# Optimization experiments

Measured on AMD Instinct MI355X. Metric: run time of the kernel, lower is better.

The kernel has to match this reference:

```python
import jax, jax.numpy as jnp
import numpy as np

TAU = 2.0      # membrane time constant
V_TH = 1.0     # spike threshold (v_reset = 0, hard reset)
T_STEPS = 4    # num_steps

@jax.custom_vjp
def heaviside_atan(x):
    # forward: Heaviside; backward: spikingjelly ATan surrogate (alpha=2)
    return (x >= 0.0).astype(x.dtype)

def _h_fwd(x):
    return heaviside_atan(x), x

def _h_bwd(x, g):
    alpha = 2.0
    return (g * (alpha / 2.0) / (1.0 + (jnp.pi / 2.0 * alpha * x) ** 2),)

heaviside_atan.defvjp(_h_fwd, _h_bwd)

def lif_multistep(x_seq):
    # spikingjelly LIFNode, step_mode='m', decay_input=True, v_reset=0, detach_reset=True
    def step(v, x):
        v = v + (x - v) / TAU                      # charge
        s = heaviside_atan(v - V_TH)               # fire (surrogate grad)
        v = v * (1.0 - jax.lax.stop_gradient(s))   # hard reset, detached spike
        return v, s
    v0 = jnp.zeros_like(x_seq[0])
    _, spikes = jax.lax.scan(step, v0, x_seq)
    return spikes

def setup_inputs() -> dict:
    key = jax.random.key(0)
    k0, k1, k2 = jax.random.split(key, 3)
    B, L, C, D, NL = 16, 512, 128, 1024, 2
    inputs = jax.random.normal(k0, (B, L, C), jnp.float32)
    enc_W = jax.random.normal(k1, (C, D), jnp.float32) / np.sqrt(C).astype(np.float32)
    enc_b = jnp.zeros((D,), jnp.float32)
    W_cells = jax.random.normal(k2, (NL, D, D), jnp.float32) / np.sqrt(D).astype(np.float32)
    b_cells = jnp.zeros((NL, D), jnp.float32)
    return {"inputs": inputs, "enc_W": enc_W, "enc_b": enc_b,
            "W_cells": W_cells, "b_cells": b_cells}

def reference(inputs, enc_W, enc_b, W_cells, b_cells):
    # temporal spike encoder: repeat input over T steps, LIF-encode to spikes
    x = jnp.swapaxes(inputs, 1, 2)                       # [B, C, L]
    x = jnp.broadcast_to(x[None], (T_STEPS,) + x.shape)  # [T, B, C, L]
    h = lif_multistep(x)
    h = jnp.swapaxes(h, -2, -1)                          # [T, B, L, C]
    # encoder linear + init LIF
    h = lif_multistep(h @ enc_W + enc_b)                 # [T, B, L, D]
    # stacked SpikeRNNCells: Linear(D,D) -> multistep LIF
    for i in range(W_cells.shape[0]):
        h = lif_multistep(h @ W_cells[i] + b_cells[i])
    out = h.mean(0)                                      # [B, L, D]
    return out, out.mean(axis=1)                         # ([B,L,D], [B,D])
```

## Files before the change

### kernel.cpp

```cpp
#include <hip/hip_runtime.h>
#include <hip/hip_bf16.h>
#include <stdint.h>

#define TSTEPS 4

typedef __bf16 bf16_t;
typedef __attribute__((ext_vector_type(8))) __bf16 bf16x8;
typedef __attribute__((ext_vector_type(16))) float f32x16;
typedef __attribute__((ext_vector_type(4))) unsigned short ushort4v;

union frag_u { bf16x8 v; uint32_t d[4]; unsigned short u[8]; };

#define WT_VM5      0xF75
#define WT_VM5_LG0  0x075
#define WT_VM4_LG0  0x074
#define WT_VM0_LG0  0x070


__global__ void spike_encode_i8(const float* __restrict__ x,
                                uint4* __restrict__ s1)
{
    const int C = 128;
    int tid = blockIdx.x * blockDim.x + threadIdx.x;
    int row = tid & 31;
    int kb  = (tid >> 5) & 7;
    int m_blk = tid >> 8;
    int m = m_blk * 32 + row;
    const float* px = x + (size_t)m * C + kb * 16;
    float xv[16];
#pragma unroll
    for (int j = 0; j < 16; j += 4) {
        float4 t4 = *(const float4*)(px + j);
        xv[j] = t4.x; xv[j+1] = t4.y; xv[j+2] = t4.z; xv[j+3] = t4.w;
    }
    float v[16];
#pragma unroll
    for (int j = 0; j < 16; ++j) v[j] = 0.0f;
#pragma unroll
    for (int t = 0; t < TSTEPS; ++t) {
        uint32_t dw[4] = {0u, 0u, 0u, 0u};
#pragma unroll
        for (int j = 0; j < 16; ++j) {
            float vv = __fadd_rn(v[j], __fmul_rn(__fsub_rn(xv[j], v[j]), 0.5f));
            bool sp = (vv >= 1.0f);
            dw[j >> 2] |= sp ? (0x3Fu << ((j & 3) * 8)) : 0u;
            v[j] = sp ? 0.0f : vv;
        }
        uint4 o; o.x = dw[0]; o.y = dw[1]; o.z = dw[2]; o.w = dw[3];
        s1[((size_t)(m_blk * 8 + kb) * 4 + t) * 32 + row] = o;
    }
}

__global__ void split_transpose_all(const float* __restrict__ enc_W,
                                    const float* __restrict__ W_cells,
                                    bf16_t* __restrict__ W1h, bf16_t* __restrict__ W1l,
                                    bf16_t* __restrict__ W2h, bf16_t* __restrict__ W2l,
                                    bf16_t* __restrict__ W3h, bf16_t* __restrict__ W3l)
{
    const int N = 1024;
    const float* W;
    bf16_t *hi, *lo;
    int K;
    if (blockIdx.z == 0) {
        if (blockIdx.x >= 4) return;
        W = enc_W; hi = W1h; lo = W1l; K = 128;
    } else if (blockIdx.z == 1) {
        W = W_cells; hi = W2h; lo = W2l; K = 1024;
    } else {
        W = W_cells + (size_t)1024 * 1024; hi = W3h; lo = W3l; K = 1024;
    }
    const int NKB = K >> 4;
    __shared__ float tile[32][33];
    int k0 = blockIdx.x * 32, n0 = blockIdx.y * 32;
    int tx = threadIdx.x & 31, ty = threadIdx.x >> 5;
    for (int kk = ty; kk < 32; kk += 8)
        tile[kk][tx] = W[(size_t)(k0 + kk) * N + n0 + tx];
    __syncthreads();

    const int nn = tx;
    const int oc = ty;
    const int o2 = oc & 3;
    const bool isLo = (oc >> 2) != 0;
    const int kblk = (k0 >> 4) + (o2 >> 1);
    const int lane_in_packet = nn + 32 * (o2 & 1);

    frag_u f;
#pragma unroll
    for (int j = 0; j < 8; ++j) {
        float wv = tile[o2 * 8 + j][nn];
        bf16_t h = (bf16_t)wv;
        bf16_t l = (bf16_t)(wv - (float)h);
        f.v[j] = isLo ? (bf16_t)(2.0f * (float)l)
                      : (bf16_t)(2.0f * (float)h);
    }
    bf16_t* dst = (isLo ? lo : hi)
        + ((size_t)((n0 + nn) >> 5) * NKB + kblk) * 512 + lane_in_packet * 8;
    *(bf16x8*)dst = f.v;
}

template <int K, bool LAST>
__global__ __launch_bounds__(256, 4)
void gemm_lif_mfma(const uint8_t* __restrict__ Abytes,
                   const bf16_t* __restrict__ Bh,
                   const bf16_t* __restrict__ Bl,
                   const float* __restrict__ bias,
                   uint8_t* __restrict__ Sbytes,
                   float* __restrict__ Out,
                   int M, int N)
{
    constexpr int NKB = K >> 4;
    __shared__ __align__(16) uint8_t ldsB[4][4096];
    __shared__ __align__(8) unsigned short sh[4][256];

    const int tid = threadIdx.x;
    const int lane = tid & 63;
    const int wid = tid >> 6;
    const int l31 = lane & 31;
    const int half = lane >> 5;

    const int bid = blockIdx.x;
    const int xcd = bid & 7;
    const int j   = bid >> 3;
    const int nh   = j >> 7;
    const int r    = j & 127;
    const int mloc = r >> 3;
    const int n_t  = nh * 8 + (r & 7);
    const int m_t  = xcd * 16 + mloc;

    const int m0 = m_t * 64, n0 = n_t * 64;
    const int wave_m = (wid & 1) * 32;
    const int wave_n = (wid >> 1) * 32;
    const int m_blk = (m0 + wave_m) >> 5;

    const uint8_t* pA = Abytes + (size_t)m_blk * NKB * 4 * 512 + l31 * 16 + half * 8;

    const uint8_t* stage_src = (const uint8_t*)(((wid & 1) ? Bl : Bh)
        + (size_t)((n0 >> 5) + (wid >> 1)) * NKB * 512) + (lane << 4);
    uint8_t* ldsStage = &ldsB[0][0] + (wid << 10);
    const uint8_t* ldsRd = &ldsB[0][0] + ((wid >> 1) << 11) + (lane << 4);

    f32x16 acc[TSTEPS];
#pragma unroll
    for (int t = 0; t < TSTEPS; ++t)
        for (int rr = 0; rr < 16; ++rr) acc[t][rr] = 0.0f;

    uint2 fm[2][4];

#define STAGE(kb_, buf_)                                                      \
    __builtin_amdgcn_global_load_lds(                                         \
        (const __attribute__((address_space(1))) uint32_t*)                   \
            (stage_src + (size_t)(kb_) * 1024),                               \
        (__attribute__((address_space(3))) uint32_t*)                         \
            (ldsStage + ((buf_) << 12)),                                      \
        16, 0, 0);

#define LOADA(kb_, s_) {                                                     \
        fm[s_][0] = *(const uint2*)(pA + ((size_t)(kb_) * 4 + 0) * 512);     \
        fm[s_][1] = *(const uint2*)(pA + ((size_t)(kb_) * 4 + 1) * 512);     \
        fm[s_][2] = *(const uint2*)(pA + ((size_t)(kb_) * 4 + 2) * 512);     \
        fm[s_][3] = *(const uint2*)(pA + ((size_t)(kb_) * 4 + 3) * 512);     \
    }

#define EXPANDF(a_, f_) {                                                    \
        (f_).d[0] = __builtin_amdgcn_perm((a_).x, 0u, 0x05000400u);          \
        (f_).d[1] = __builtin_amdgcn_perm((a_).x, 0u, 0x07000600u);          \
        (f_).d[2] = __builtin_amdgcn_perm((a_).y, 0u, 0x05000400u);          \
        (f_).d[3] = __builtin_amdgcn_perm((a_).y, 0u, 0x07000600u);          \
    }

#define MFMAS(s_, fhv_, flv_) {                                              \
        frag_u af0, af1, af2, af3;                                           \
        EXPANDF(fm[s_][0], af0);                                             \
        EXPANDF(fm[s_][1], af1);                                             \
        EXPANDF(fm[s_][2], af2);                                             \
        EXPANDF(fm[s_][3], af3);                                             \
        acc[0] = __builtin_amdgcn_mfma_f32_32x32x16_bf16(af0.v, fhv_, acc[0], 0, 0, 0); \
        acc[1] = __builtin_amdgcn_mfma_f32_32x32x16_bf16(af1.v, fhv_, acc[1], 0, 0, 0); \
        acc[2] = __builtin_amdgcn_mfma_f32_32x32x16_bf16(af2.v, fhv_, acc[2], 0, 0, 0); \
        acc[3] = __builtin_amdgcn_mfma_f32_32x32x16_bf16(af3.v, fhv_, acc[3], 0, 0, 0); \
        acc[0] = __builtin_amdgcn_mfma_f32_32x32x16_bf16(af0.v, flv_, acc[0], 0, 0, 0); \
        acc[1] = __builtin_amdgcn_mfma_f32_32x32x16_bf16(af1.v, flv_, acc[1], 0, 0, 0); \
        acc[2] = __builtin_amdgcn_mfma_f32_32x32x16_bf16(af2.v, flv_, acc[2], 0, 0, 0); \
        acc[3] = __builtin_amdgcn_mfma_f32_32x32x16_bf16(af3.v, flv_, acc[3], 0, 0, 0); \
    }

#define STEPD(kb_, p_) {                                                     \
        STAGE((kb_) + 2, ((kb_) + 2) & 3);                                   \
        LOADA((kb_) + 1, (p_) ^ 1);                                          \
        __builtin_amdgcn_s_waitcnt(WT_VM5_LG0);                              \
        asm volatile("" ::: "memory");                                       \
        MFMAS(p_, cfh, cfl);                                                 \
        __builtin_amdgcn_s_barrier();                                        \
        asm volatile("" ::: "memory");                                       \
        cfh = *(const bf16x8*)(ldsRd + ((((kb_) + 1) & 3) << 12));           \
        cfl = *(const bf16x8*)(ldsRd + ((((kb_) + 1) & 3) << 12) + 1024);    \
    }

    STAGE(0, 0);
    STAGE(1, 1);
    LOADA(0, 0);
    __builtin_amdgcn_s_waitcnt(WT_VM5);
    asm volatile("" ::: "memory");
    __builtin_amdgcn_s_barrier();
    asm volatile("" ::: "memory");
    bf16x8 cfh = *(const bf16x8*)(ldsRd);
    bf16x8 cfl = *(const bf16x8*)(ldsRd + 1024);

    for (int kb = 0; kb < NKB - 2; kb += 2) {
        STEPD(kb + 0, 0);
        STEPD(kb + 1, 1);
    }
    LOADA(NKB - 1, 1);
    __builtin_amdgcn_s_waitcnt(WT_VM4_LG0);
    asm volatile("" ::: "memory");
    MFMAS(0, cfh, cfl);
    __builtin_amdgcn_s_barrier();
    asm volatile("" ::: "memory");
    cfh = *(const bf16x8*)(ldsRd + (((NKB - 1) & 3) << 12));
    cfl = *(const bf16x8*)(ldsRd + (((NKB - 1) & 3) << 12) + 1024);
    __builtin_amdgcn_s_waitcnt(WT_VM0_LG0);
    asm volatile("" ::: "memory");
    MFMAS(1, cfh, cfl);

#undef STEPD
#undef MFMAS
#undef EXPANDF
#undef LOADA
#undef STAGE

    const float bv = bias[n0 + wave_n + l31];
    f32x16 vmem;
#pragma unroll
    for (int rr = 0; rr < 16; ++rr) vmem[rr] = 0.0f;
    uint64_t bits = 0ull;
    unsigned short* myt = &sh[wid][0];

    const int NKBo = N >> 4;
    const int kbase = (n0 + wave_n) >> 4;

    for (int t = 0; t < TSTEPS; ++t) {
#pragma unroll
        for (int rr = 0; rr < 16; ++rr) {
            float y = __fadd_rn(acc[t][rr], bv);
            float vv = vmem[rr];
            vv = __fadd_rn(vv, __fmul_rn(__fsub_rn(y, vv), 0.5f));
            bool sp = (vv >= 1.0f);
            vmem[rr] = sp ? 0.0f : vv;
            if (LAST) {
                bits |= sp ? (1ull << (rr * 4 + t)) : 0ull;
            } else {
                unsigned long long b = __ballot(sp);
                if (l31 == 0) {
                    uint32_t hb = (uint32_t)(b >> (half * 32));
                    int rowi = (rr & 3) + 8 * (rr >> 2) + 4 * half;
                    myt[(rowi * 2 + 0) * 4 + t] = (unsigned short)hb;
                    myt[(rowi * 2 + 1) * 4 + t] = (unsigned short)(hb >> 16);
                }
            }
        }
    }

    if (LAST) {
        float psum = 0.0f;
#pragma unroll
        for (int rr = 0; rr < 16; ++rr) {
            int m_r = (rr & 3) + 8 * (rr >> 2) + 4 * half;
            int m = m0 + wave_m + m_r;
            int n = n0 + wave_n + l31;
            int cnt = __popc((unsigned)((bits >> (rr * 4)) & 0xFull));
            float val = 0.25f * (float)cnt;
            Out[(size_t)m * N + n] = val;
            psum += val;
        }
        psum += __shfl_xor(psum, 32, 64);
        if (half == 0) {
            float* out2 = Out + (size_t)M * N;
            int b = m0 >> 9;
            int n = n0 + wave_n + l31;
            atomicAdd(out2 + (size_t)b * N + n, psum * (1.0f / 512.0f));
        }
    } else {
        const ushort4v pk = *(const ushort4v*)&myt[(l31 * 2 + half) * 4];
#pragma unroll
        for (int t = 0; t < TSTEPS; ++t) {
            uint32_t m16 = pk[t];
            uint4 o;
            o.x = (((m16      ) & 0xFu) * 0x00204081u & 0x01010101u) * 0x3Fu;
            o.y = (((m16 >>  4) & 0xFu) * 0x00204081u & 0x01010101u) * 0x3Fu;
            o.z = (((m16 >>  8) & 0xFu) * 0x00204081u & 0x01010101u) * 0x3Fu;
            o.w = (((m16 >> 12) & 0xFu) * 0x00204081u & 0x01010101u) * 0x3Fu;
            *(uint4*)(Sbytes + ((((size_t)m_blk * NKBo + kbase + half) * 4 + t)
                                * 32 + l31) * 16) = o;
        }
    }
}

__global__ void zero_out2(float* __restrict__ out2, int n)
{
    int i = blockIdx.x * blockDim.x + threadIdx.x;
    if (i < n) out2[i] = 0.0f;
}

extern "C" void kernel_launch(void* const* d_in, const int* in_sizes, int n_in,
                              void* d_out, int out_size, void* d_ws, size_t ws_size,
                              hipStream_t stream)
{
    const float* inputs  = (const float*)d_in[0];
    const float* enc_W   = (const float*)d_in[1];
    const float* enc_b   = (const float*)d_in[2];
    const float* W_cells = (const float*)d_in[3];
    const float* b_cells = (const float*)d_in[4];

    const int B = 16, L = 512, C = 128, D = 1024;
    const int M = B * L;

    char* ws = (char*)d_ws;
    size_t off = 0;
    uint8_t* s1 = (uint8_t*)(ws + off);
    off += (size_t)(M / 32) * (C / 16) * 4 * 32 * 16;
    bf16_t* W1h = (bf16_t*)(ws + off); off += (size_t)C * D * 2;
    bf16_t* W1l = (bf16_t*)(ws + off); off += (size_t)C * D * 2;
    bf16_t* W2h = (bf16_t*)(ws + off); off += (size_t)D * D * 2;
    bf16_t* W2l = (bf16_t*)(ws + off); off += (size_t)D * D * 2;
    bf16_t* W3h = (bf16_t*)(ws + off); off += (size_t)D * D * 2;
    bf16_t* W3l = (bf16_t*)(ws + off); off += (size_t)D * D * 2;
    uint8_t* h0 = (uint8_t*)(ws + off);
    off += (size_t)(M / 32) * (D / 16) * 4 * 32 * 16;
    uint8_t* h1 = (uint8_t*)(ws + off);

    float* out  = (float*)d_out;
    float* out2 = out + (size_t)M * D;

    split_transpose_all<<<dim3(32, 32, 3), 256, 0, stream>>>(
        enc_W, W_cells, W1h, W1l, W2h, W2l, W3h, W3l);

    spike_encode_i8<<<256, 256, 0, stream>>>(inputs, (uint4*)s1);

    zero_out2<<<(B * D + 255) / 256, 256, 0, stream>>>(out2, B * D);

    const int nblocks = (M / 64) * (D / 64);
    gemm_lif_mfma<128, false><<<nblocks, 256, 0, stream>>>(
        s1, W1h, W1l, enc_b, h0, nullptr, M, D);
    gemm_lif_mfma<1024, false><<<nblocks, 256, 0, stream>>>(
        h0, W2h, W2l, b_cells, h1, nullptr, M, D);
    gemm_lif_mfma<1024, true><<<nblocks, 256, 0, stream>>>(
        h1, W3h, W3l, b_cells + D, nullptr, out, M, D);
}
```

Before: 303.2 us.

## Process two K-blocks per barrier phase with deeper 8-slot LDS ring

Result: no change. 307.7 us (+1.5%).

```diff
diff --git a/kernel.cpp b/kernel.cpp
--- a/kernel.cpp
+++ b/kernel.cpp
@@ -11,9 +11,9 @@
 
 union frag_u { bf16x8 v; uint32_t d[4]; unsigned short u[8]; };
 
-#define WT_VM5      0xF75
-#define WT_VM5_LG0  0x075
-#define WT_VM4_LG0  0x074
+#define WT_VM10_LG0 0x07A
+#define WT_VM8_LG0  0x078
+#define WT_VM10     0xF7A
 #define WT_VM0_LG0  0x070
 
 
@@ -99,7 +99,7 @@
 }
 
 template <int K, bool LAST>
-__global__ __launch_bounds__(256, 4)
+__global__ __launch_bounds__(256, 3)
 void gemm_lif_mfma(const uint8_t* __restrict__ Abytes,
                    const bf16_t* __restrict__ Bh,
                    const bf16_t* __restrict__ Bl,
@@ -109,7 +109,8 @@
                    int M, int N)
 {
     constexpr int NKB = K >> 4;
-    __shared__ __align__(16) uint8_t ldsB[4][4096];
+    constexpr int NP  = NKB >> 1;
+    __shared__ __align__(16) uint8_t ldsB[8][4096];
     __shared__ __align__(8) unsigned short sh[4][256];
 
     const int tid = threadIdx.x;
@@ -144,21 +145,33 @@
     for (int t = 0; t < TSTEPS; ++t)
         for (int rr = 0; rr < 16; ++rr) acc[t][rr] = 0.0f;
 
-    uint2 fm[2][4];
-
-#define STAGE(kb_, buf_)                                                      \
+    uint2 fm[2][2][4];
+    bf16x8 cfh0, cfl0, cfh1, cfl1;
+
+#define STAGE1(kb_)                                                           \
     __builtin_amdgcn_global_load_lds(                                         \
         (const __attribute__((address_space(1))) uint32_t*)                   \
             (stage_src + (size_t)(kb_) * 1024),                               \
         (__attribute__((address_space(3))) uint32_t*)                         \
-            (ldsStage + ((buf_) << 12)),                                      \
+            (ldsStage + (((kb_) & 7) << 12)),                                 \
         16, 0, 0);
 
-#define LOADA(kb_, s_) {                                                     \
-        fm[s_][0] = *(const uint2*)(pA + ((size_t)(kb_) * 4 + 0) * 512);     \
-        fm[s_][1] = *(const uint2*)(pA + ((size_t)(kb_) * 4 + 1) * 512);     \
-        fm[s_][2] = *(const uint2*)(pA + ((size_t)(kb_) * 4 + 2) * 512);     \
-        fm[s_][3] = *(const uint2*)(pA + ((size_t)(kb_) * 4 + 3) * 512);     \
+#define LOADA2(kb_, s_) {                                                    \
+        fm[s_][0][0] = *(const uint2*)(pA + ((size_t)(kb_) * 4 + 0) * 512);  \
+        fm[s_][0][1] = *(const uint2*)(pA + ((size_t)(kb_) * 4 + 1) * 512);  \
+        fm[s_][0][2] = *(const uint2*)(pA + ((size_t)(kb_) * 4 + 2) * 512);  \
+        fm[s_][0][3] = *(const uint2*)(pA + ((size_t)(kb_) * 4 + 3) * 512);  \
+        fm[s_][1][0] = *(const uint2*)(pA + ((size_t)(kb_) * 4 + 4) * 512);  \
+        fm[s_][1][1] = *(const uint2*)(pA + ((size_t)(kb_) * 4 + 5) * 512);  \
+        fm[s_][1][2] = *(const uint2*)(pA + ((size_t)(kb_) * 4 + 6) * 512);  \
+        fm[s_][1][3] = *(const uint2*)(pA + ((size_t)(kb_) * 4 + 7) * 512);  \
+    }
+
+#define FRAGRD(kb_) {                                                        \
+        cfh0 = *(const bf16x8*)(ldsRd + (((kb_) & 7) << 12));                \
+        cfl0 = *(const bf16x8*)(ldsRd + (((kb_) & 7) << 12) + 1024);         \
+        cfh1 = *(const bf16x8*)(ldsRd + ((((kb_) + 1) & 7) << 12));          \
+        cfl1 = *(const bf16x8*)(ldsRd + ((((kb_) + 1) & 7) << 12) + 1024);   \
     }
 
 #define EXPANDF(a_, f_) {                                                    \
@@ -168,12 +181,12 @@
         (f_).d[3] = __builtin_amdgcn_perm((a_).y, 0u, 0x07000600u);          \
     }
 
-#define MFMAS(s_, fhv_, flv_) {                                              \
+#define MFMAS(s_, i_, fhv_, flv_) {                                          \
         frag_u af0, af1, af2, af3;                                           \
-        EXPANDF(fm[s_][0], af0);                                             \
-        EXPANDF(fm[s_][1], af1);                                             \
-        EXPANDF(fm[s_][2], af2);                                             \
-        EXPANDF(fm[s_][3], af3);                                             \
+        EXPANDF(fm[s_][i_][0], af0);                                         \
+        EXPANDF(fm[s_][i_][1], af1);                                         \
+        EXPANDF(fm[s_][i_][2], af2);                                         \
+        EXPANDF(fm[s_][i_][3], af3);                                         \
         acc[0] = __builtin_amdgcn_mfma_f32_32x32x16_bf16(af0.v, fhv_, acc[0], 0, 0, 0); \
         acc[1] = __builtin_amdgcn_mfma_f32_32x32x16_bf16(af1.v, fhv_, acc[1], 0, 0, 0); \
         acc[2] = __builtin_amdgcn_mfma_f32_32x32x16_bf16(af2.v, fhv_, acc[2], 0, 0, 0); \
@@ -184,49 +197,50 @@
         acc[3] = __builtin_amdgcn_mfma_f32_32x32x16_bf16(af3.v, flv_, acc[3], 0, 0, 0); \
     }
 
-#define STEPD(kb_, p_) {                                                     \
-        STAGE((kb_) + 2, ((kb_) + 2) & 3);                                   \
-        LOADA((kb_) + 1, (p_) ^ 1);                                          \
-        __builtin_amdgcn_s_waitcnt(WT_VM5_LG0);                              \
+#define PHASE(p_, s_) {                                                      \
+        STAGE1(2 * (p_) + 4);                                                \
+        STAGE1(2 * (p_) + 5);                                                \
+        LOADA2(2 * (p_) + 2, (s_) ^ 1);                                      \
+        __builtin_amdgcn_s_waitcnt(WT_VM10_LG0);                             \
         asm volatile("" ::: "memory");                                       \
-        MFMAS(p_, cfh, cfl);                                                 \
+        MFMAS(s_, 0, cfh0, cfl0);                                            \
+        MFMAS(s_, 1, cfh1, cfl1);                                            \
         __builtin_amdgcn_s_barrier();                                        \
         asm volatile("" ::: "memory");                                       \
-        cfh = *(const bf16x8*)(ldsRd + ((((kb_) + 1) & 3) << 12));           \
-        cfl = *(const bf16x8*)(ldsRd + ((((kb_) + 1) & 3) << 12) + 1024);    \
-    }
-
-    STAGE(0, 0);
-    STAGE(1, 1);
-    LOADA(0, 0);
-    __builtin_amdgcn_s_waitcnt(WT_VM5);
+        FRAGRD(2 * (p_) + 2);                                                \
+    }
+
+    STAGE1(0); STAGE1(1); STAGE1(2); STAGE1(3);
+    LOADA2(0, 0);
+    __builtin_amdgcn_s_waitcnt(WT_VM10);
     asm volatile("" ::: "memory");
     __builtin_amdgcn_s_barrier();
     asm volatile("" ::: "memory");
-    bf16x8 cfh = *(const bf16x8*)(ldsRd);
-    bf16x8 cfl = *(const bf16x8*)(ldsRd + 1024);
-
-    for (int kb = 0; kb < NKB - 2; kb += 2) {
-        STEPD(kb + 0, 0);
-        STEPD(kb + 1, 1);
-    }
-    LOADA(NKB - 1, 1);
-    __builtin_amdgcn_s_waitcnt(WT_VM4_LG0);
-    asm volatile("" ::: "memory");
-    MFMAS(0, cfh, cfl);
+    FRAGRD(0);
+
+    for (int p = 0; p < NP - 2; p += 2) {
+        PHASE(p + 0, 0);
+        PHASE(p + 1, 1);
+    }
+    LOADA2(NKB - 2, 1);
+    __builtin_amdgcn_s_waitcnt(WT_VM8_LG0);
+    asm volatile("" ::: "memory");
+    MFMAS(0, 0, cfh0, cfl0);
+    MFMAS(0, 1, cfh1, cfl1);
     __builtin_amdgcn_s_barrier();
     asm volatile("" ::: "memory");
-    cfh = *(const bf16x8*)(ldsRd + (((NKB - 1) & 3) << 12));
-    cfl = *(const bf16x8*)(ldsRd + (((NKB - 1) & 3) << 12) + 1024);
+    FRAGRD(NKB - 2);
     __builtin_amdgcn_s_waitcnt(WT_VM0_LG0);
     asm volatile("" ::: "memory");
-    MFMAS(1, cfh, cfl);
-
-#undef STEPD
+    MFMAS(1, 0, cfh0, cfl0);
+    MFMAS(1, 1, cfh1, cfl1);
+
+#undef PHASE
 #undef MFMAS
 #undef EXPANDF
-#undef LOADA
-#undef STAGE
+#undef FRAGRD
+#undef LOADA2
+#undef STAGE1
 
     const float bv = bias[n0 + wave_n + l31];
     f32x16 vmem;
```

## Stage spike A-operand through LDS ring alongside B instead of direct global loads

Applied to the files above, without the earlier changes.

Result: faster. 279.3 us (-7.9%).

```diff
diff --git a/kernel.cpp b/kernel.cpp
--- a/kernel.cpp
+++ b/kernel.cpp
@@ -11,9 +11,9 @@
 
 union frag_u { bf16x8 v; uint32_t d[4]; unsigned short u[8]; };
 
-#define WT_VM5      0xF75
-#define WT_VM5_LG0  0x075
-#define WT_VM4_LG0  0x074
+#define WT_VM2_LG0  0x072
+#define WT_VM2      0xF72
+#define WT_LG0      0xC07F
 #define WT_VM0_LG0  0x070
 
 
@@ -109,7 +109,7 @@
                    int M, int N)
 {
     constexpr int NKB = K >> 4;
-    __shared__ __align__(16) uint8_t ldsB[4][4096];
+    __shared__ __align__(16) uint8_t ldsR[4][8192];
     __shared__ __align__(8) unsigned short sh[4][256];
 
     const int tid = threadIdx.x;
@@ -132,33 +132,62 @@
     const int wave_n = (wid >> 1) * 32;
     const int m_blk = (m0 + wave_m) >> 5;
 
-    const uint8_t* pA = Abytes + (size_t)m_blk * NKB * 4 * 512 + l31 * 16 + half * 8;
-
-    const uint8_t* stage_src = (const uint8_t*)(((wid & 1) ? Bl : Bh)
-        + (size_t)((n0 >> 5) + (wid >> 1)) * NKB * 512) + (lane << 4);
-    uint8_t* ldsStage = &ldsB[0][0] + (wid << 10);
-    const uint8_t* ldsRd = &ldsB[0][0] + ((wid >> 1) << 11) + (lane << 4);
+    const uint8_t* src0;
+    const uint8_t* src1;
+    int sstride, d0off, d1off;
+    if (wid < 2) {
+        const uint8_t* base = Abytes + ((size_t)(m0 >> 5) + wid) * NKB * 2048;
+        src0 = base + (lane << 4);
+        src1 = base + 1024 + (lane << 4);
+        sstride = 2048;
+        d0off = wid * 2048;
+        d1off = d0off + 1024;
+    } else {
+        const int nl = wid - 2;
+        src0 = (const uint8_t*)(Bh + ((size_t)(n0 >> 5) + nl) * NKB * 512)
+               + (lane << 4);
+        src1 = (const uint8_t*)(Bl + ((size_t)(n0 >> 5) + nl) * NKB * 512)
+               + (lane << 4);
+        sstride = 1024;
+        d0off = 4096 + nl * 2048;
+        d1off = d0off + 1024;
+    }
+    uint8_t* ringBase = &ldsR[0][0];
+
+    const int aRdOff = (wid & 1) * 2048 + l31 * 16 + half * 8;
+    const int bRdOff = 4096 + ((wid >> 1) << 11) + (lane << 4);
 
     f32x16 acc[TSTEPS];
 #pragma unroll
     for (int t = 0; t < TSTEPS; ++t)
         for (int rr = 0; rr < 16; ++rr) acc[t][rr] = 0.0f;
 
-    uint2 fm[2][4];
-
-#define STAGE(kb_, buf_)                                                      \
+    uint2 fm[4];
+    bf16x8 cfh, cfl;
+
+#define STAGE2(kb_) {                                                         \
     __builtin_amdgcn_global_load_lds(                                         \
         (const __attribute__((address_space(1))) uint32_t*)                   \
-            (stage_src + (size_t)(kb_) * 1024),                               \
+            (src0 + (size_t)(kb_) * sstride),                                 \
         (__attribute__((address_space(3))) uint32_t*)                         \
-            (ldsStage + ((buf_) << 12)),                                      \
-        16, 0, 0);
-
-#define LOADA(kb_, s_) {                                                     \
-        fm[s_][0] = *(const uint2*)(pA + ((size_t)(kb_) * 4 + 0) * 512);     \
-        fm[s_][1] = *(const uint2*)(pA + ((size_t)(kb_) * 4 + 1) * 512);     \
-        fm[s_][2] = *(const uint2*)(pA + ((size_t)(kb_) * 4 + 2) * 512);     \
-        fm[s_][3] = *(const uint2*)(pA + ((size_t)(kb_) * 4 + 3) * 512);     \
+            (ringBase + (((kb_) & 3) << 13) + d0off),                         \
+        16, 0, 0);                                                            \
+    __builtin_amdgcn_global_load_lds(                                         \
+        (const __attribute__((address_space(1))) uint32_t*)                   \
+            (src1 + (size_t)(kb_) * sstride),                                 \
+        (__attribute__((address_space(3))) uint32_t*)                         \
+            (ringBase + (((kb_) & 3) << 13) + d1off),                         \
+        16, 0, 0);                                                            \
+    }
+
+#define FRAGRD(kb_) {                                                        \
+        const uint8_t* sb = ringBase + (((kb_) & 3) << 13);                  \
+        fm[0] = *(const uint2*)(sb + aRdOff);                                \
+        fm[1] = *(const uint2*)(sb + aRdOff + 512);                          \
+        fm[2] = *(const uint2*)(sb + aRdOff + 1024);                         \
+        fm[3] = *(const uint2*)(sb + aRdOff + 1536);                         \
+        cfh = *(const bf16x8*)(sb + bRdOff);                                 \
+        cfl = *(const bf16x8*)(sb + bRdOff + 1024);                          \
     }
 
 #define EXPANDF(a_, f_) {                                                    \
@@ -168,65 +197,53 @@
         (f_).d[3] = __builtin_amdgcn_perm((a_).y, 0u, 0x07000600u);          \
     }
 
-#define MFMAS(s_, fhv_, flv_) {                                              \
+#define MFMAS() {                                                            \
         frag_u af0, af1, af2, af3;                                           \
-        EXPANDF(fm[s_][0], af0);                                             \
-        EXPANDF(fm[s_][1], af1);                                             \
-        EXPANDF(fm[s_][2], af2);                                             \
-        EXPANDF(fm[s_][3], af3);                                             \
-        acc[0] = __builtin_amdgcn_mfma_f32_32x32x16_bf16(af0.v, fhv_, acc[0], 0, 0, 0); \
-        acc[1] = __builtin_amdgcn_mfma_f32_32x32x16_bf16(af1.v, fhv_, acc[1], 0, 0, 0); \
-        acc[2] = __builtin_amdgcn_mfma_f32_32x32x16_bf16(af2.v, fhv_, acc[2], 0, 0, 0); \
-        acc[3] = __builtin_amdgcn_mfma_f32_32x32x16_bf16(af3.v, fhv_, acc[3], 0, 0, 0); \
-        acc[0] = __builtin_amdgcn_mfma_f32_32x32x16_bf16(af0.v, flv_, acc[0], 0, 0, 0); \
-        acc[1] = __builtin_amdgcn_mfma_f32_32x32x16_bf16(af1.v, flv_, acc[1], 0, 0, 0); \
-        acc[2] = __builtin_amdgcn_mfma_f32_32x32x16_bf16(af2.v, flv_, acc[2], 0, 0, 0); \
-        acc[3] = __builtin_amdgcn_mfma_f32_32x32x16_bf16(af3.v, flv_, acc[3], 0, 0, 0); \
-    }
-
-#define STEPD(kb_, p_) {                                                     \
-        STAGE((kb_) + 2, ((kb_) + 2) & 3);                                   \
-        LOADA((kb_) + 1, (p_) ^ 1);                                          \
-        __builtin_amdgcn_s_waitcnt(WT_VM5_LG0);                              \
-        asm volatile("" ::: "memory");                                       \
-        MFMAS(p_, cfh, cfl);                                                 \
-        __builtin_amdgcn_s_barrier();                                        \
-        asm volatile("" ::: "memory");                                       \
-        cfh = *(const bf16x8*)(ldsRd + ((((kb_) + 1) & 3) << 12));           \
-        cfl = *(const bf16x8*)(ldsRd + ((((kb_) + 1) & 3) << 12) + 1024);    \
-    }
-
-    STAGE(0, 0);
-    STAGE(1, 1);
-    LOADA(0, 0);
-    __builtin_amdgcn_s_waitcnt(WT_VM5);
+        EXPANDF(fm[0], af0);                                                 \
+        EXPANDF(fm[1], af1);                                                 \
+        EXPANDF(fm[2], af2);                                                 \
+        EXPANDF(fm[3], af3);                                                 \
+        acc[0] = __builtin_amdgcn_mfma_f32_32x32x16_bf16(af0.v, cfh, acc[0], 0, 0, 0); \
+        acc[1] = __builtin_amdgcn_mfma_f32_32x32x16_bf16(af1.v, cfh, acc[1], 0, 0, 0); \
+        acc[2] = __builtin_amdgcn_mfma_f32_32x32x16_bf16(af2.v, cfh, acc[2], 0, 0, 0); \
+        acc[3] = __builtin_amdgcn_mfma_f32_32x32x16_bf16(af3.v, cfh, acc[3], 0, 0, 0); \
+        acc[0] = __builtin_amdgcn_mfma_f32_32x32x16_bf16(af0.v, cfl, acc[0], 0, 0, 0); \
+        acc[1] = __builtin_amdgcn_mfma_f32_32x32x16_bf16(af1.v, cfl, acc[1], 0, 0, 0); \
+        acc[2] = __builtin_amdgcn_mfma_f32_32x32x16_bf16(af2.v, cfl, acc[2], 0, 0, 0); \
+        acc[3] = __builtin_amdgcn_mfma_f32_32x32x16_bf16(af3.v, cfl, acc[3], 0, 0, 0); \
+    }
+
+    STAGE2(0);
+    STAGE2(1);
+    __builtin_amdgcn_s_waitcnt(WT_VM2);
     asm volatile("" ::: "memory");
     __builtin_amdgcn_s_barrier();
     asm volatile("" ::: "memory");
-    bf16x8 cfh = *(const bf16x8*)(ldsRd);
-    bf16x8 cfl = *(const bf16x8*)(ldsRd + 1024);
-
-    for (int kb = 0; kb < NKB - 2; kb += 2) {
-        STEPD(kb + 0, 0);
-        STEPD(kb + 1, 1);
-    }
-    LOADA(NKB - 1, 1);
-    __builtin_amdgcn_s_waitcnt(WT_VM4_LG0);
-    asm volatile("" ::: "memory");
-    MFMAS(0, cfh, cfl);
+    FRAGRD(0);
+
+    for (int kb = 0; kb < NKB - 2; ++kb) {
+        STAGE2(kb + 2);
+        __builtin_amdgcn_s_waitcnt(WT_VM2_LG0);
+        asm volatile("" ::: "memory");
+        MFMAS();
+        __builtin_amdgcn_s_barrier();
+        asm volatile("" ::: "memory");
+        FRAGRD(kb + 1);
+    }
+    __builtin_amdgcn_s_waitcnt(WT_VM0_LG0);
+    asm volatile("" ::: "memory");
+    MFMAS();
     __builtin_amdgcn_s_barrier();
     asm volatile("" ::: "memory");
-    cfh = *(const bf16x8*)(ldsRd + (((NKB - 1) & 3) << 12));
-    cfl = *(const bf16x8*)(ldsRd + (((NKB - 1) & 3) << 12) + 1024);
-    __builtin_amdgcn_s_waitcnt(WT_VM0_LG0);
-    asm volatile("" ::: "memory");
-    MFMAS(1, cfh, cfl);
-
-#undef STEPD
+    FRAGRD(NKB - 1);
+    __builtin_amdgcn_s_waitcnt(WT_LG0);
+    asm volatile("" ::: "memory");
+    MFMAS();
+
 #undef MFMAS
 #undef EXPANDF
-#undef LOADA
-#undef STAGE
+#undef FRAGRD
+#undef STAGE2
 
     const float bv = bias[n0 + wave_n + l31];
     f32x16 vmem;
```
